# Performance work log

Hardware: AMD Instinct MI355X
Metric: run time of the kernel (lower is better)

The kernel has to match this reference:

```python
import jax, jax.numpy as jnp
import numpy as np

B, N, C, H = 32, 577, 768, 12
D = C // H  # head_dim = 64


def _rotate_half(t):
    half = t.shape[-1] // 2
    return jnp.concatenate([-t[..., half:], t[..., :half]], axis=-1)


def _rope(t, sin, cos):
    # t: [B, H, N-1, D]; sin/cos: [N-1, D] broadcast over batch and heads
    return t * cos + _rotate_half(t) * sin


def setup_inputs() -> dict:
    key = jax.random.key(0)
    ks = jax.random.split(key, 5)
    x = jax.random.normal(ks[0], (B, N, C), dtype=jnp.float32)
    w_qkv = jax.random.normal(ks[1], (C, 3 * C), dtype=jnp.float32) * (1.0 / np.sqrt(C))
    b_qkv = jnp.zeros((3 * C,), dtype=jnp.float32)
    w_proj = jax.random.normal(ks[2], (C, C), dtype=jnp.float32) * (1.0 / np.sqrt(C))
    b_proj = jnp.zeros((C,), dtype=jnp.float32)
    # rotary tables for the N-1 non-CLS tokens
    pos = jnp.arange(N - 1, dtype=jnp.float32)[:, None]            # [N-1, 1]
    inv_freq = 1.0 / (10000.0 ** (jnp.arange(0, D, 2, dtype=jnp.float32) / D))  # [D/2]
    ang = pos * inv_freq[None, :]                                   # [N-1, D/2]
    ang = jnp.concatenate([ang, ang], axis=-1)                      # [N-1, D]
    rope_sin = jnp.sin(ang)
    rope_cos = jnp.cos(ang)
    return {"x": x, "w_qkv": w_qkv, "b_qkv": b_qkv, "w_proj": w_proj,
            "b_proj": b_proj, "rope_sin": rope_sin, "rope_cos": rope_cos}


def reference(x, w_qkv, b_qkv, w_proj, b_proj, rope_sin, rope_cos):
    Bx, Nx, Cx = x.shape
    qkv = x @ w_qkv + b_qkv                                   # [B, N, 3C]
    qkv = qkv.reshape(Bx, Nx, 3, H, D).transpose(2, 0, 3, 1, 4)  # [3, B, H, N, D]
    q, k, v = qkv[0], qkv[1], qkv[2]
    # RoPE only on non-CLS tokens (index 0 is CLS)
    q = jnp.concatenate([q[:, :, :1, :], _rope(q[:, :, 1:, :], rope_sin, rope_cos)], axis=2)
    k = jnp.concatenate([k[:, :, :1, :], _rope(k[:, :, 1:, :], rope_sin, rope_cos)], axis=2)
    q = q / jnp.sqrt(jnp.float32(D))
    attn = jnp.einsum("bhqd,bhkd->bhqk", q, k)               # [B, H, N, N]
    attn = jax.nn.softmax(attn.astype(jnp.float32), axis=-1).astype(x.dtype)
    out = jnp.einsum("bhqk,bhkd->bhqd", attn, v)             # [B, H, N, D]
    out = out.transpose(0, 2, 1, 3).reshape(Bx, Nx, Cx)       # [B, N, C]
    return out @ w_proj + b_proj
```

## Files before the change

kernel.cpp:

```cpp
#include <hip/hip_runtime.h>

#define Bdim 32
#define Ndim 577
#define Cdim 768
#define Hdim 12
#define Ddim 64
#define Mdim (Bdim*Ndim)
#define VSTRIDE 640
#define TSTRIDE 152
#define QSCALE 0.18033688f
#define MGRP 19

typedef __attribute__((ext_vector_type(4))) float f32x4;
typedef __attribute__((ext_vector_type(8))) __bf16 bf16x8;
typedef __attribute__((ext_vector_type(4))) __bf16 bf16x4;

__device__ __forceinline__ void gl_lds16(const __bf16* g, __bf16* l) {
  __builtin_amdgcn_global_load_lds((const __attribute__((address_space(1))) void*)g,
                                   (__attribute__((address_space(3))) void*)l, 16, 0, 0);
}

__global__ __launch_bounds__(256) void f32_to_bf16(const float4* __restrict__ in,
                                                   bf16x4* __restrict__ out, int n4) {
  int i = blockIdx.x * 256 + threadIdx.x;
  if (i < n4) {
    float4 v = in[i];
    bf16x4 o = {(__bf16)v.x, (__bf16)v.y, (__bf16)v.z, (__bf16)v.w};
    out[i] = o;
  }
}

__global__ __launch_bounds__(256) void transpose_f32_wfrag(const float* __restrict__ in,
                                                           __bf16* __restrict__ out,
                                                           int Cc) {
  __shared__ float tile[64][65];
  int bx = blockIdx.x * 64;
  int by = blockIdx.y * 64;
  int tx = threadIdx.x & 63, ty = threadIdx.x >> 6;
  #pragma unroll
  for (int i = ty; i < 64; i += 4)
    tile[i][tx] = in[(size_t)(by + i) * Cc + bx + tx];
  __syncthreads();
  #pragma unroll
  for (int it = 0; it < 2; ++it) {
    int idx = it * 256 + threadIdx.x;
    int nl = idx & 63, kc = idx >> 6;
    bf16x8 o;
    #pragma unroll
    for (int j = 0; j < 8; ++j) o[j] = (__bf16)tile[kc * 8 + j][nl];
    int n = bx + nl, kk = by + kc * 8;
    *(bf16x8*)(out + ((size_t)(n >> 4) * 96 + (kk >> 3)) * 128 + (n & 15) * 8) = o;
  }
}

__device__ __forceinline__ void gemm_split_core(const __bf16* __restrict__ A,
                                                const __bf16* __restrict__ WF,
                                                int m0, int n0,
                                                __bf16* As, f32x4 acc[4][4]) {
  const int t = threadIdx.x;
  const int lane = t & 63, w = t >> 6;
  const int quad = lane >> 4, l16 = lane & 15;
  const int wm = w >> 1, wn = w & 1;
  const int nb16 = (n0 >> 4) + wn * 4;

  for (int k0 = 0; k0 < 768; k0 += 64) {
    __syncthreads();
    bf16x8 b[2][4];
    #pragma unroll
    for (int s = 0; s < 2; ++s)
      #pragma unroll
      for (int i = 0; i < 4; ++i)
        b[s][i] = *(const bf16x8*)(WF +
            ((size_t)(nb16 + i) * 96 + (k0 >> 3) + s * 4 + quad) * 128 + l16 * 8);
    #pragma unroll
    for (int e = 0; e < 4; ++e) {
      int h = e >> 1;
      int j = ((e & 1) << 2) | w;
      int row = j * 16 + (lane >> 2);
      int col = k0 + h * 32 + (lane & 3) * 8;
      int ar = m0 + row; if (ar > Mdim - 1) ar = Mdim - 1;
      gl_lds16(A + (size_t)ar * 768 + col, As + h * 4096 + j * 512 + lane * 8);
    }
    __syncthreads();
    #pragma unroll
    for (int s = 0; s < 2; ++s) {
      bf16x8 a[4];
      #pragma unroll
      for (int i = 0; i < 4; ++i)
        a[i] = *(const bf16x8*)(As + s * 4096 + (wm * 64 + i * 16 + l16) * 32 + quad * 8);
      #pragma unroll
      for (int mt = 0; mt < 4; ++mt)
        #pragma unroll
        for (int nt = 0; nt < 4; ++nt)
          acc[mt][nt] = __builtin_amdgcn_mfma_f32_16x16x32_bf16(a[mt], b[s][nt], acc[mt][nt], 0, 0, 0);
    }
  }
}

__device__ __forceinline__ bool xcd_decode(int lin, int nb, int mb, int& n, int& m) {
  int x8 = lin & 7;
  int rest = lin >> 3;
  n = rest % nb;
  int mg = rest / nb;
  m = mg * 8 + x8;
  return m < mb;
}

__global__ __launch_bounds__(256) void qk_kernel(const __bf16* __restrict__ x,
                                                 const __bf16* __restrict__ wf,
                                                 const float* __restrict__ b_qkv,
                                                 const float* __restrict__ rs,
                                                 const float* __restrict__ rc,
                                                 __bf16* __restrict__ q,
                                                 __bf16* __restrict__ k) {
  __shared__ __bf16 As[2 * 128 * 32];
  int nb, mbk;
  if (!xcd_decode(blockIdx.x, 12, 145, nb, mbk)) return;
  const int n0 = nb * 128, m0 = mbk * 128;

  f32x4 acc[4][4];
  const f32x4 fz = {0.f, 0.f, 0.f, 0.f};
  for (int i = 0; i < 4; ++i) for (int j = 0; j < 4; ++j) acc[i][j] = fz;
  gemm_split_core(x, wf, m0, n0, As, acc);

  const int lane = threadIdx.x & 63, w = threadIdx.x >> 6;
  const int quad = lane >> 4, l16 = lane & 15;
  const int wm = w >> 1, wn = w & 1;
  const int colbase = n0 + wn * 64;
  const int matrix = colbase / 768;
  const int head = (colbase % 768) / 64;

  #pragma unroll
  for (int mt = 0; mt < 4; ++mt) {
    int mbase = m0 + wm * 64 + mt * 16 + quad * 4;
    #pragma unroll
    for (int r = 0; r < 4; ++r) {
      int m = mbase + r;
      if (m >= Mdim) continue;
      int bb = m / 577, tok = m % 577;
      #pragma unroll
      for (int nt = 0; nt < 4; ++nt) {
        int d = nt * 16 + l16;
        float val = acc[mt][nt][r] + b_qkv[colbase + d];
        if (tok > 0) {
          float partner = acc[mt][nt ^ 2][r] + b_qkv[colbase + (d ^ 32)];
          float sn = rs[(size_t)(tok - 1) * 64 + d];
          float cs = rc[(size_t)(tok - 1) * 64 + d];
          float rot = (d < 32) ? -partner : partner;
          val = val * cs + rot * sn;
        }
        __bf16* dst;
        if (matrix == 0) { val *= QSCALE; dst = q; } else dst = k;
        dst[((size_t)(bb * 12 + head) * 577 + tok) * 64 + d] = (__bf16)val;
      }
    }
  }
}

__global__ __launch_bounds__(256) void v_kernel(const __bf16* __restrict__ x,
                                                const __bf16* __restrict__ wf,
                                                const float* __restrict__ b_qkv,
                                                __bf16* __restrict__ vt) {
  __shared__ __bf16 As[2 * 128 * 32];
  __shared__ __bf16 Ts[64 * TSTRIDE];
  int nb, mbk;
  if (!xcd_decode(blockIdx.x, 6, 145, nb, mbk)) return;
  const int n0 = 1536 + nb * 128, m0 = mbk * 128;

  f32x4 acc[4][4];
  const f32x4 fz = {0.f, 0.f, 0.f, 0.f};
  for (int i = 0; i < 4; ++i) for (int j = 0; j < 4; ++j) acc[i][j] = fz;
  gemm_split_core(x, wf, m0, n0, As, acc);

  const int t = threadIdx.x;
  const int lane = t & 63, w = t >> 6;
  const int quad = lane >> 4, l16 = lane & 15;
  const int wm = w >> 1, wn = w & 1;
  const int colbase = n0 + wn * 64;

  #pragma unroll
  for (int h = 0; h < 2; ++h) {
    __syncthreads();
    if (wn == h) {
      #pragma unroll
      for (int mt = 0; mt < 4; ++mt) {
        int tokbase = wm * 64 + mt * 16 + quad * 4;
        #pragma unroll
        for (int r = 0; r < 4; ++r) {
          #pragma unroll
          for (int nt = 0; nt < 4; ++nt) {
            int dl = nt * 16 + l16;
            Ts[dl * TSTRIDE + tokbase + r] =
                (__bf16)(acc[mt][nt][r] + b_qkv[colbase + dl]);
          }
        }
      }
    }
    __syncthreads();
    int hh = (n0 + h * 64 - 1536) / 64;
    #pragma unroll
    for (int it = 0; it < 4; ++it) {
      int c = it * 256 + t;
      int dl = c >> 4, chunk = c & 15;
      bf16x8 vv = *(const bf16x8*)(Ts + dl * TSTRIDE + chunk * 8);
      #pragma unroll
      for (int j = 0; j < 8; ++j) {
        int m = m0 + chunk * 8 + j;
        if (m < Mdim) {
          int bb = m / 577, tok = m % 577;
          vt[((size_t)(bb * 12 + hh) * 64 + dl) * VSTRIDE + tok] = vv[j];
        }
      }
    }
  }
}

__global__ __launch_bounds__(256) void attn_kernel(const __bf16* __restrict__ q,
                                                   const __bf16* __restrict__ k,
                                                   const __bf16* __restrict__ vt,
                                                   __bf16* __restrict__ ao) {
  __shared__ __bf16 ks[4096];
  __shared__ __bf16 vs[4096];
  __shared__ __bf16 ps[64 * 72];

  const int x8 = blockIdx.x & 7;
  const int rest = blockIdx.x >> 3;
  const int qp = rest % 5;
  const int bh = (rest / 5) * 8 + x8;

  const int t = threadIdx.x;
  const int lane = t & 63, w = t >> 6;
  const int quad = lane >> 4, l16 = lane & 15;

  const __bf16* qbase = q + (size_t)bh * 577 * 64;
  const __bf16* kbase = k + (size_t)bh * 577 * 64;
  const __bf16* vbase = vt + (size_t)bh * 64 * VSTRIDE;

  bf16x8 aq[2][2];
  #pragma unroll
  for (int qi = 0; qi < 2; ++qi)
    #pragma unroll
    for (int s = 0; s < 2; ++s)
      aq[qi][s] = *(const bf16x8*)(qbase +
          (size_t)(qp * 128 + qi * 64 + w * 16 + l16) * 64 + (s * 4 + quad) * 8);

  bf16x8 kreg[2], vreg[2];
  #pragma unroll
  for (int p = 0; p < 2; ++p) {
    int g = p * 256 + t;
    kreg[p] = *(const bf16x8*)(kbase + (size_t)(g & 63) * 64 + (g >> 6) * 8);
    vreg[p] = *(const bf16x8*)(vbase + (size_t)(g & 63) * VSTRIDE + (g >> 6) * 8);
  }

  f32x4 O[2][4]; const f32x4 fz = {0.f, 0.f, 0.f, 0.f};
  for (int qi = 0; qi < 2; ++qi) for (int i = 0; i < 4; ++i) O[qi][i] = fz;
  float l_part[2][4] = {{0.f, 0.f, 0.f, 0.f}, {0.f, 0.f, 0.f, 0.f}};

  for (int kt = 0; kt < 10; ++kt) {
    __syncthreads();
    #pragma unroll
    for (int p = 0; p < 2; ++p) {
      int g = p * 256 + t;
      *(bf16x8*)(ks + (size_t)g * 8) = kreg[p];
      *(bf16x8*)(vs + (size_t)g * 8) = vreg[p];
    }
    __syncthreads();

    if (kt < 9) {
      #pragma unroll
      for (int p = 0; p < 2; ++p) {
        int g = p * 256 + t;
        kreg[p] = *(const bf16x8*)(kbase + (size_t)((kt + 1) * 64 + (g & 63)) * 64 + (g >> 6) * 8);
        vreg[p] = *(const bf16x8*)(vbase + (size_t)(g & 63) * VSTRIDE + (kt + 1) * 64 + (g >> 6) * 8);
      }
      __builtin_amdgcn_sched_barrier(0);
    }

    int kv_left = 577 - kt * 64;

    #pragma unroll
    for (int qi = 0; qi < 2; ++qi) {
      f32x4 S[4]; for (int i = 0; i < 4; ++i) S[i] = fz;
      __builtin_amdgcn_s_setprio(1);
      #pragma unroll
      for (int s = 0; s < 2; ++s) {
        #pragma unroll
        for (int nt = 0; nt < 4; ++nt) {
          bf16x8 b = *(const bf16x8*)(ks + (size_t)((s * 4 + quad) * 64 + nt * 16 + l16) * 8);
          S[nt] = __builtin_amdgcn_mfma_f32_16x16x32_bf16(aq[qi][s], b, S[nt], 0, 0, 0);
        }
      }
      __builtin_amdgcn_s_setprio(0);

      if (kv_left < 64) {
        #pragma unroll
        for (int nt = 0; nt < 4; ++nt) {
          int c = nt * 16 + l16;
          if (c >= kv_left) { S[nt][0] = -1e30f; S[nt][1] = -1e30f; S[nt][2] = -1e30f; S[nt][3] = -1e30f; }
        }
      }

      #pragma unroll
      for (int r = 0; r < 4; ++r) {
        #pragma unroll
        for (int nt = 0; nt < 4; ++nt) {
          float e = exp2f(S[nt][r]);
          l_part[qi][r] += e;
          ps[(size_t)(w * 16 + quad * 4 + r) * 72 + nt * 16 + l16] = (__bf16)e;
        }
      }

      __builtin_amdgcn_s_setprio(1);
      #pragma unroll
      for (int s = 0; s < 2; ++s) {
        bf16x8 a = *(const bf16x8*)(ps + (size_t)(w * 16 + l16) * 72 + s * 32 + quad * 8);
        #pragma unroll
        for (int dt = 0; dt < 4; ++dt) {
          bf16x8 b = *(const bf16x8*)(vs + (size_t)((s * 4 + quad) * 64 + dt * 16 + l16) * 8);
          O[qi][dt] = __builtin_amdgcn_mfma_f32_16x16x32_bf16(a, b, O[qi][dt], 0, 0, 0);
        }
      }
      __builtin_amdgcn_s_setprio(0);
    }
  }

  const int bb = bh / 12, hh = bh % 12;
  #pragma unroll
  for (int qi = 0; qi < 2; ++qi) {
    const int qrow0 = qp * 128 + qi * 64 + w * 16 + quad * 4;
    #pragma unroll
    for (int r = 0; r < 4; ++r) {
      float l = l_part[qi][r];
      l += __shfl_xor(l, 1); l += __shfl_xor(l, 2);
      l += __shfl_xor(l, 4); l += __shfl_xor(l, 8);
      int row = qrow0 + r;
      if (row < 577) {
        float inv = 1.f / l;
        size_t base = ((size_t)(bb * 577 + row)) * 768 + hh * 64;
        #pragma unroll
        for (int dt = 0; dt < 4; ++dt)
          ao[base + dt * 16 + l16] = (__bf16)(O[qi][dt][r] * inv);
      }
    }
  }
}

__global__ __launch_bounds__(256) void proj_kernel(const __bf16* __restrict__ ao,
                                                   const __bf16* __restrict__ wprojF,
                                                   const float* __restrict__ b_proj,
                                                   float* __restrict__ out) {
  __shared__ __bf16 As[2 * 128 * 32];
  int nb, mbk;
  if (!xcd_decode(blockIdx.x, 6, 145, nb, mbk)) return;
  const int n0 = nb * 128, m0 = mbk * 128;

  f32x4 acc[4][4];
  const f32x4 fz = {0.f, 0.f, 0.f, 0.f};
  for (int i = 0; i < 4; ++i) for (int j = 0; j < 4; ++j) acc[i][j] = fz;
  gemm_split_core(ao, wprojF, m0, n0, As, acc);

  const int lane = threadIdx.x & 63, w = threadIdx.x >> 6;
  const int quad = lane >> 4, l16 = lane & 15;
  const int wm = w >> 1, wn = w & 1;
  const int colbase = n0 + wn * 64;

  #pragma unroll
  for (int mt = 0; mt < 4; ++mt) {
    int mbase = m0 + wm * 64 + mt * 16 + quad * 4;
    #pragma unroll
    for (int r = 0; r < 4; ++r) {
      int m = mbase + r;
      if (m >= Mdim) continue;
      #pragma unroll
      for (int nt = 0; nt < 4; ++nt) {
        int c = colbase + nt * 16 + l16;
        out[(size_t)m * 768 + c] = acc[mt][nt][r] + b_proj[c];
      }
    }
  }
}

extern "C" void kernel_launch(void* const* d_in, const int* in_sizes, int n_in,
                              void* d_out, int out_size, void* d_ws, size_t ws_size,
                              hipStream_t stream) {
  const float* x      = (const float*)d_in[0];
  const float* w_qkv  = (const float*)d_in[1];
  const float* b_qkv  = (const float*)d_in[2];
  const float* w_proj = (const float*)d_in[3];
  const float* b_proj = (const float*)d_in[4];
  const float* rsn    = (const float*)d_in[5];
  const float* rcs    = (const float*)d_in[6];
  float* out = (float*)d_out;

  constexpr size_t QK_E = (size_t)Bdim * Hdim * Ndim * Ddim;
  constexpr size_t VT_E = (size_t)Bdim * Hdim * Ddim * VSTRIDE;
  constexpr size_t AO_E = (size_t)Mdim * Cdim;
  __bf16* q      = (__bf16*)d_ws;
  __bf16* k      = q + QK_E;
  __bf16* vt     = k + QK_E;
  __bf16* ao     = vt + VT_E;
  __bf16* xb     = ao;
  __bf16* wqkvF  = ao + AO_E;
  __bf16* wprojF = wqkvF + (size_t)2304 * 768;

  f32_to_bf16<<<13848, 256, 0, stream>>>((const float4*)x, (bf16x4*)xb,
                                         (int)(AO_E / 4));
  transpose_f32_wfrag<<<dim3(36, 12), 256, 0, stream>>>(w_qkv, wqkvF, 2304);
  transpose_f32_wfrag<<<dim3(12, 12), 256, 0, stream>>>(w_proj, wprojF, 768);
  qk_kernel<<<8 * MGRP * 12, 256, 0, stream>>>(xb, wqkvF, b_qkv, rsn, rcs, q, k);
  v_kernel<<<8 * MGRP * 6, 256, 0, stream>>>(xb, wqkvF, b_qkv, vt);
  attn_kernel<<<1920, 256, 0, stream>>>(q, k, vt, ao);
  proj_kernel<<<8 * MGRP * 6, 256, 0, stream>>>(ao, wprojF, b_proj, out);
}
```

Before: 418.9 us.

## Widen GEMM tiles to 128x256 with 512 threads and merge prep kernels

The three preprocessing kernels (x to bf16, two weight transposes) are merged into one launch that dispatches on block index. The QKV and projection GEMMs now use 512-thread blocks with 8 waves arranged 2x4, each covering a 128x256 output tile, so each A tile in LDS serves twice as many columns. This halves the number of GEMM blocks and the redundant A-tile loads, at the cost of fewer blocks for load balancing and a larger per-block footprint.

```diff
diff --git a/kernel.cpp b/kernel.cpp
--- a/kernel.cpp
+++ b/kernel.cpp
@@ -20,22 +20,10 @@
                                    (__attribute__((address_space(3))) void*)l, 16, 0, 0);
 }
 
-__global__ __launch_bounds__(256) void f32_to_bf16(const float4* __restrict__ in,
-                                                   bf16x4* __restrict__ out, int n4) {
-  int i = blockIdx.x * 256 + threadIdx.x;
-  if (i < n4) {
-    float4 v = in[i];
-    bf16x4 o = {(__bf16)v.x, (__bf16)v.y, (__bf16)v.z, (__bf16)v.w};
-    out[i] = o;
-  }
-}
-
-__global__ __launch_bounds__(256) void transpose_f32_wfrag(const float* __restrict__ in,
-                                                           __bf16* __restrict__ out,
-                                                           int Cc) {
-  __shared__ float tile[64][65];
-  int bx = blockIdx.x * 64;
-  int by = blockIdx.y * 64;
+__device__ __forceinline__ void wfrag_body(const float* __restrict__ in,
+                                           __bf16* __restrict__ out,
+                                           int Cc, int bx, int by,
+                                           float (*tile)[65]) {
   int tx = threadIdx.x & 63, ty = threadIdx.x >> 6;
   #pragma unroll
   for (int i = ty; i < 64; i += 4)
@@ -50,6 +38,31 @@
     for (int j = 0; j < 8; ++j) o[j] = (__bf16)tile[kc * 8 + j][nl];
     int n = bx + nl, kk = by + kc * 8;
     *(bf16x8*)(out + ((size_t)(n >> 4) * 96 + (kk >> 3)) * 128 + (n & 15) * 8) = o;
+  }
+}
+
+#define NCONV 13848
+__global__ __launch_bounds__(256) void prep_kernel(const float4* __restrict__ x4,
+                                                   bf16x4* __restrict__ xb4, int n4,
+                                                   const float* __restrict__ wqkv,
+                                                   __bf16* __restrict__ wqkvF,
+                                                   const float* __restrict__ wproj,
+                                                   __bf16* __restrict__ wprojF) {
+  __shared__ float tile[64][65];
+  int b = blockIdx.x;
+  if (b < NCONV) {
+    int i = b * 256 + threadIdx.x;
+    if (i < n4) {
+      float4 v = x4[i];
+      bf16x4 o = {(__bf16)v.x, (__bf16)v.y, (__bf16)v.z, (__bf16)v.w};
+      xb4[i] = o;
+    }
+  } else if (b < NCONV + 432) {
+    int r = b - NCONV;
+    wfrag_body(wqkv, wqkvF, 2304, (r % 36) * 64, (r / 36) * 64, tile);
+  } else {
+    int r = b - NCONV - 432;
+    wfrag_body(wproj, wprojF, 768, (r % 12) * 64, (r / 12) * 64, tile);
   }
 }
 
@@ -60,7 +73,7 @@
   const int t = threadIdx.x;
   const int lane = t & 63, w = t >> 6;
   const int quad = lane >> 4, l16 = lane & 15;
-  const int wm = w >> 1, wn = w & 1;
+  const int wm = w >> 2, wn = w & 3;
   const int nb16 = (n0 >> 4) + wn * 4;
 
   for (int k0 = 0; k0 < 768; k0 += 64) {
@@ -73,13 +86,15 @@
         b[s][i] = *(const bf16x8*)(WF +
             ((size_t)(nb16 + i) * 96 + (k0 >> 3) + s * 4 + quad) * 128 + l16 * 8);
     #pragma unroll
-    for (int e = 0; e < 4; ++e) {
-      int h = e >> 1;
-      int j = ((e & 1) << 2) | w;
-      int row = j * 16 + (lane >> 2);
-      int col = k0 + h * 32 + (lane & 3) * 8;
+    for (int e = 0; e < 2; ++e) {
+      int g = e * 512 + t;
+      int h = g >> 9;
+      int j = (g >> 6) & 7;
+      int gl = g & 63;
+      int row = j * 16 + (gl >> 2);
+      int col = k0 + h * 32 + (gl & 3) * 8;
       int ar = m0 + row; if (ar > Mdim - 1) ar = Mdim - 1;
-      gl_lds16(A + (size_t)ar * 768 + col, As + h * 4096 + j * 512 + lane * 8);
+      gl_lds16(A + (size_t)ar * 768 + col, As + h * 4096 + j * 512 + gl * 8);
     }
     __syncthreads();
     #pragma unroll
@@ -106,7 +121,7 @@
   return m < mb;
 }
 
-__global__ __launch_bounds__(256) void qk_kernel(const __bf16* __restrict__ x,
+__global__ __launch_bounds__(512) void qk_kernel(const __bf16* __restrict__ x,
                                                  const __bf16* __restrict__ wf,
                                                  const float* __restrict__ b_qkv,
                                                  const float* __restrict__ rs,
@@ -115,8 +130,8 @@
                                                  __bf16* __restrict__ k) {
   __shared__ __bf16 As[2 * 128 * 32];
   int nb, mbk;
-  if (!xcd_decode(blockIdx.x, 12, 145, nb, mbk)) return;
-  const int n0 = nb * 128, m0 = mbk * 128;
+  if (!xcd_decode(blockIdx.x, 6, 145, nb, mbk)) return;
+  const int n0 = nb * 256, m0 = mbk * 128;
 
   f32x4 acc[4][4];
   const f32x4 fz = {0.f, 0.f, 0.f, 0.f};
@@ -125,7 +140,7 @@
 
   const int lane = threadIdx.x & 63, w = threadIdx.x >> 6;
   const int quad = lane >> 4, l16 = lane & 15;
-  const int wm = w >> 1, wn = w & 1;
+  const int wm = w >> 2, wn = w & 3;
   const int colbase = n0 + wn * 64;
   const int matrix = colbase / 768;
   const int head = (colbase % 768) / 64;
@@ -157,15 +172,15 @@
   }
 }
 
-__global__ __launch_bounds__(256) void v_kernel(const __bf16* __restrict__ x,
+__global__ __launch_bounds__(512) void v_kernel(const __bf16* __restrict__ x,
                                                 const __bf16* __restrict__ wf,
                                                 const float* __restrict__ b_qkv,
                                                 __bf16* __restrict__ vt) {
   __shared__ __bf16 As[2 * 128 * 32];
   __shared__ __bf16 Ts[64 * TSTRIDE];
   int nb, mbk;
-  if (!xcd_decode(blockIdx.x, 6, 145, nb, mbk)) return;
-  const int n0 = 1536 + nb * 128, m0 = mbk * 128;
+  if (!xcd_decode(blockIdx.x, 3, 145, nb, mbk)) return;
+  const int n0 = 1536 + nb * 256, m0 = mbk * 128;
 
   f32x4 acc[4][4];
   const f32x4 fz = {0.f, 0.f, 0.f, 0.f};
@@ -175,11 +190,11 @@
   const int t = threadIdx.x;
   const int lane = t & 63, w = t >> 6;
   const int quad = lane >> 4, l16 = lane & 15;
-  const int wm = w >> 1, wn = w & 1;
+  const int wm = w >> 2, wn = w & 3;
   const int colbase = n0 + wn * 64;
 
   #pragma unroll
-  for (int h = 0; h < 2; ++h) {
+  for (int h = 0; h < 4; ++h) {
     __syncthreads();
     if (wn == h) {
       #pragma unroll
@@ -197,10 +212,10 @@
       }
     }
     __syncthreads();
-    int hh = (n0 + h * 64 - 1536) / 64;
-    #pragma unroll
-    for (int it = 0; it < 4; ++it) {
-      int c = it * 256 + t;
+    int hh = (n0 - 1536) / 64 + h;
+    #pragma unroll
+    for (int it = 0; it < 2; ++it) {
+      int c = it * 512 + t;
       int dl = c >> 4, chunk = c & 15;
       bf16x8 vv = *(const bf16x8*)(Ts + dl * TSTRIDE + chunk * 8);
       #pragma unroll
@@ -345,14 +360,14 @@
   }
 }
 
-__global__ __launch_bounds__(256) void proj_kernel(const __bf16* __restrict__ ao,
+__global__ __launch_bounds__(512) void proj_kernel(const __bf16* __restrict__ ao,
                                                    const __bf16* __restrict__ wprojF,
                                                    const float* __restrict__ b_proj,
                                                    float* __restrict__ out) {
   __shared__ __bf16 As[2 * 128 * 32];
   int nb, mbk;
-  if (!xcd_decode(blockIdx.x, 6, 145, nb, mbk)) return;
-  const int n0 = nb * 128, m0 = mbk * 128;
+  if (!xcd_decode(blockIdx.x, 3, 145, nb, mbk)) return;
+  const int n0 = nb * 256, m0 = mbk * 128;
 
   f32x4 acc[4][4];
   const f32x4 fz = {0.f, 0.f, 0.f, 0.f};
@@ -361,7 +376,7 @@
 
   const int lane = threadIdx.x & 63, w = threadIdx.x >> 6;
   const int quad = lane >> 4, l16 = lane & 15;
-  const int wm = w >> 1, wn = w & 1;
+  const int wm = w >> 2, wn = w & 3;
   const int colbase = n0 + wn * 64;
 
   #pragma unroll
@@ -403,12 +418,11 @@
   __bf16* wqkvF  = ao + AO_E;
   __bf16* wprojF = wqkvF + (size_t)2304 * 768;
 
-  f32_to_bf16<<<13848, 256, 0, stream>>>((const float4*)x, (bf16x4*)xb,
-                                         (int)(AO_E / 4));
-  transpose_f32_wfrag<<<dim3(36, 12), 256, 0, stream>>>(w_qkv, wqkvF, 2304);
-  transpose_f32_wfrag<<<dim3(12, 12), 256, 0, stream>>>(w_proj, wprojF, 768);
-  qk_kernel<<<8 * MGRP * 12, 256, 0, stream>>>(xb, wqkvF, b_qkv, rsn, rcs, q, k);
-  v_kernel<<<8 * MGRP * 6, 256, 0, stream>>>(xb, wqkvF, b_qkv, vt);
+  prep_kernel<<<NCONV + 432 + 144, 256, 0, stream>>>(
+      (const float4*)x, (bf16x4*)xb, (int)(AO_E / 4),
+      w_qkv, wqkvF, w_proj, wprojF);
+  qk_kernel<<<8 * MGRP * 6, 512, 0, stream>>>(xb, wqkvF, b_qkv, rsn, rcs, q, k);
+  v_kernel<<<8 * MGRP * 3, 512, 0, stream>>>(xb, wqkvF, b_qkv, vt);
   attn_kernel<<<1920, 256, 0, stream>>>(q, k, vt, ao);
-  proj_kernel<<<8 * MGRP * 6, 256, 0, stream>>>(ao, wprojF, b_proj, out);
-}
+  proj_kernel<<<8 * MGRP * 3, 512, 0, stream>>>(ao, wprojF, b_proj, out);
+}
```

Result: slower. 476.2 us (+13.7%).
